# Optimization experiments

Measured on AMD Instinct MI355X. Metric: run time of the kernel, lower is better.

## Reference

```python
import jax, jax.numpy as jnp
import numpy as np

# dims
B, NO, NE = 32, 100, 600          # batch, img objects, img edges
NK, KE, L = 1000, 1000, 8         # kg entities, kg edges, token len
R = 8                              # reasoning-program nodes
H, IMG, LOC = 512, 2048, 5        # hidden, img feat, loc feat
EMB, V, MID, C = 300, 10000, 512, 3000
PAD = 1


def lang_encode(tokens, embed, W, b):
    # masked mean-pool of word embeddings + projection (LanguageEncoder)
    m = (tokens != PAD).astype(jnp.float32)            # [B,N,L]
    e = embed[tokens]                                   # [B,N,L,EMB]
    pooled = (e * m[..., None]).sum(-2) / jnp.maximum(m.sum(-1, keepdims=True), 1.0)
    return jnp.tanh(pooled @ W + b)                     # [B,N,H]


def find_attn(q, k, mask, Wq, Wk, v):
    # Find module: additive attention of program-node queries over key set
    qp = q @ Wq                                         # [B,R,MID]
    kp = k @ Wk                                         # [B,N,MID]
    s = jnp.einsum('brnm,m->brn', jnp.tanh(qp[:, :, None, :] + kp[:, None, :, :]), v)
    if mask is not None:
        s = jnp.where(mask[:, None, :], s, -1e9)
    return jax.nn.softmax(s, axis=-1)                   # [B,R,N] attention maps


def setup_inputs():
    key = jax.random.key(0)
    ks = jax.random.split(key, 30)
    w = lambda i, shp: jax.random.normal(ks[i], shp, jnp.float32) * 0.05
    inp = {
        'img_feat': jax.random.normal(ks[0], (B, NO, IMG), jnp.float32),
        'img_loc': jax.random.uniform(ks[1], (B, NO, LOC), jnp.float32),
        'img_node1_id_list': jax.random.randint(ks[2], (B, NE), 0, NO),
        'img_node2_id_list': jax.random.randint(ks[3], (B, NE), 0, NO),
        'kg_entity': jax.random.randint(ks[4], (B, NK, L), 0, V),
        'kg_e1_ids_list': jax.random.randint(ks[5], (B, KE), 0, NK),
        'kg_e2_ids_list': jax.random.randint(ks[6], (B, KE), 0, NK),
        'kg_edge': jax.random.randint(ks[7], (B, KE, L), 0, V),
        'r_nodes': jax.random.randint(ks[8], (B, R, L), 0, V),
        'r_connects': jax.random.randint(ks[9], (B, R), 0, R),
        'r_type': jax.random.randint(ks[10], (B, R), 0, 3),
        'embed': w(11, (V, EMB)),
        'W_lang': w(12, (EMB, H)), 'b_lang': jnp.zeros((H,), jnp.float32),
        'W_img': w(13, (IMG, H)), 'b_img': jnp.zeros((H,), jnp.float32),
        'W_loc': w(14, (LOC, H)), 'b_loc': jnp.zeros((H,), jnp.float32),
        'W_rel': w(15, (2 * H, H)), 'b_rel': jnp.zeros((H,), jnp.float32),
        'Wq_n': w(16, (H, MID)), 'Wk_n': w(17, (H, MID)), 'v_n': w(18, (MID,)),
        'Wq_e': w(19, (H, MID)), 'Wk_e': w(20, (H, MID)), 'v_e': w(21, (MID,)),
        'W1': w(22, (H, MID)), 'b1': jnp.zeros((MID,), jnp.float32),
        'W2': w(23, (MID, C)), 'b2': jnp.zeros((C,), jnp.float32),
    }
    return inp


def reference(img_feat, img_loc, img_node1_id_list, img_node2_id_list, kg_entity,
              kg_e1_ids_list, kg_e2_ids_list, kg_edge, r_nodes, r_connects, r_type,
              embed, W_lang, b_lang, W_img, b_img, W_loc, b_loc, W_rel, b_rel,
              Wq_n, Wk_n, v_n, Wq_e, Wk_e, v_e, W1, b1, W2, b2):
    # --- image graph features ---
    img_f = img_feat @ W_img + b_img                    # [B,NO,H]
    img_node_feat = img_f + (img_loc @ W_loc + b_loc)
    n1 = jnp.take_along_axis(img_f, img_node1_id_list[..., None], axis=1)  # [B,NE,H]
    n2 = jnp.take_along_axis(img_f, img_node2_id_list[..., None], axis=1)
    img_edge_feat = jnp.concatenate([n1, n2], -1) @ W_rel + b_rel          # [B,NE,H]
    # --- kg graph features ---
    kg_node_feat = lang_encode(kg_entity, embed, W_lang, b_lang)           # [B,NK,H]
    kg_node_mask = jnp.any(kg_entity != PAD, axis=-1)                      # [B,NK]
    kg_edge_feat = lang_encode(kg_edge, embed, W_lang, b_lang)             # [B,KE,H]
    # --- reasoning-program node features ---
    r_feat = lang_encode(r_nodes, embed, W_lang, b_lang)                   # [B,R,H]
    # --- Find over nodes (img + kg entities) ---
    node_keys = jnp.concatenate([img_node_feat, kg_node_feat], axis=1)     # [B,NO+NK,H]
    node_mask = jnp.concatenate([jnp.ones((B, NO), bool), kg_node_mask], axis=1)
    all_map = find_attn(r_feat, node_keys, node_mask, Wq_n, Wk_n, v_n)     # [B,R,NO+NK]
    node_re = jnp.einsum('brn,bnh->brh', all_map, node_keys)               # grounded node feats
    # --- Find over edges (img + kg relations) ---
    edge_keys = jnp.concatenate([img_edge_feat, kg_edge_feat], axis=1)     # [B,NE+KE,H]
    edge_map = find_attn(r_feat, edge_keys, None, Wq_e, Wk_e, v_e)
    edge_ctx = jnp.einsum('brn,bnh->brh', edge_map, edge_keys)
    # --- Reason head on root program node ---
    final = node_re[:, -1] + edge_ctx[:, -1]                               # [B,H]
    return jnp.tanh(final @ W1 + b1) @ W2 + b2                             # [B,C]
```

## Files before the change

kernel.cpp:

```cpp
#include <hip/hip_runtime.h>
#include <hip/hip_bf16.h>
#include <math.h>

#define B_   32
#define NO_  100
#define NE_  600
#define NK_  1000
#define KE_  1000
#define L_   8
#define R_   8
#define H_   512
#define IMG_ 2048
#define LOC_ 5
#define EMB_ 300
#define MID_ 512
#define C_   3000
#define PAD_ 1

#define NN_  (NO_ + NK_)
#define NEK_ (NE_ + KE_)

typedef __attribute__((ext_vector_type(8))) short bf16x8;
typedef __attribute__((ext_vector_type(4))) float f32x4;

__device__ __forceinline__ float4 ldf4(const float* p) { return *(const float4*)p; }

__device__ __forceinline__ float bf2f(short s) {
    unsigned u = ((unsigned)(unsigned short)s) << 16;
    float f; __builtin_memcpy(&f, &u, 4); return f;
}
__device__ __forceinline__ short f2bf(float f) {
    unsigned u; __builtin_memcpy(&u, &f, 4);
    u = (u + 0x7fffu + ((u >> 16) & 1u)) >> 16;
    return (short)u;
}

__device__ __forceinline__ long tiled_off(int row, int k, int KSa) {
    return ((((long)(row >> 7) * KSa + (k >> 5)) * 4 + ((k >> 3) & 3)) << 10)
           + ((long)(row & 127) << 3) + (k & 7);
}

__device__ __forceinline__ void gload16(const void* g, void* l) {
    __builtin_amdgcn_global_load_lds(
        (__attribute__((address_space(1))) void*)(g),
        (__attribute__((address_space(3))) void*)(l), 16, 0, 0);
}

__global__ __launch_bounds__(256) void wprep_kernel(
    const float* __restrict__ W, short* __restrict__ Wp, int K, int KS)
{
    int idx = blockIdx.x * 256 + threadIdx.x;
    int total = 4 * KS * 4 * 128;
    if (idx >= total) return;
    int nl = idx & 127;
    int kg = (idx >> 7) & 3;
    int t  = idx >> 9;
    int ks = t % KS;
    int nb = t / KS;
    int n = nb * 128 + nl;
    short o[8];
#pragma unroll
    for (int j = 0; j < 8; ++j) {
        int k = ks * 32 + kg * 8 + j;
        o[j] = (k < K) ? f2bf(W[(long)k * H_ + n]) : (short)0;
    }
    *(uint4*)&Wp[(long)idx * 8] = *(uint4*)o;
}

__global__ __launch_bounds__(256) void cvt_bf16_kernel(
    const float* __restrict__ src, short* __restrict__ dst, long n)
{
    long i = ((long)blockIdx.x * 256 + threadIdx.x) * 8;
    if (i >= n) return;
    float4 a = ldf4(src + i), b = ldf4(src + i + 4);
    short o[8] = { f2bf(a.x), f2bf(a.y), f2bf(a.z), f2bf(a.w),
                   f2bf(b.x), f2bf(b.y), f2bf(b.z), f2bf(b.w) };
    *(uint4*)&dst[i] = *(uint4*)o;
}

__global__ __launch_bounds__(256) void cvt_tiled_kernel(
    const float* __restrict__ src, short* __restrict__ dst, int K, long ngroups)
{
    long g = (long)blockIdx.x * 256 + threadIdx.x;
    if (g >= ngroups) return;
    int perRow = K >> 3;
    int row = (int)(g / perRow);
    int k   = (int)(g - (long)row * perRow) * 8;
    const float* p = src + (long)row * K + k;
    float4 a = ldf4(p), b = ldf4(p + 4);
    short o[8] = { f2bf(a.x), f2bf(a.y), f2bf(a.z), f2bf(a.w),
                   f2bf(b.x), f2bf(b.y), f2bf(b.z), f2bf(b.w) };
    *(uint4*)&dst[tiled_off(row, k, K >> 5)] = *(uint4*)o;
}

__global__ __launch_bounds__(256) void pool_kernel(
    const int* __restrict__ tokA, const int* __restrict__ tokB, int split,
    int tok_stride, int tok_off, const short* __restrict__ embed_bf,
    short* __restrict__ pooled, float* __restrict__ maskout, int nrows)
{
    __shared__ int   toks[32][8];
    __shared__ float rinv[32];
    int tid = threadIdx.x, base = blockIdx.x * 32;
    const int* tokens; int local;
    if (base < split) { tokens = tokA; local = base; }
    else              { tokens = tokB; local = base - split; }
    {
        int r = tid >> 3, t = tid & 7;
        int i = base + r;
        toks[r][t] = (i < nrows) ? tokens[tok_off + (long)(local + r) * tok_stride + t] : PAD_;
    }
    __syncthreads();
    if (tid < 32) {
        int c = 0;
#pragma unroll
        for (int t = 0; t < 8; ++t) c += (toks[tid][t] != PAD_);
        rinv[tid] = 1.0f / fmaxf((float)c, 1.0f);
        int i = base + tid;
        if (maskout && i < split && i < nrows) maskout[i] = (c > 0) ? 1.0f : 0.0f;
    }
    __syncthreads();

    for (int task = tid; task < 32 * 40; task += 256) {
        int r = task / 40, kg = task - r * 40;
        float s[8] = {0.f,0.f,0.f,0.f,0.f,0.f,0.f,0.f};
        if (kg < 38) {
#pragma unroll
            for (int t = 0; t < 8; ++t) {
                int tok = toks[r][t];
                if (tok != PAD_) {
                    bf16x8 e = *(const bf16x8*)&embed_bf[(long)tok * EMB_ + kg * 8];
#pragma unroll
                    for (int j = 0; j < 8; ++j) s[j] += bf2f(e[j]);
                }
            }
        }
        float iv = rinv[r];
        short o[8];
#pragma unroll
        for (int j = 0; j < 8; ++j) {
            float v = s[j] * iv;
            if (kg == 37 && j >= 4) v = 0.f;
            o[j] = f2bf(v);
        }
        *(uint4*)&pooled[tiled_off(base + r, kg * 8, 10)] = *(uint4*)o;
    }
}

template<int DUAL>
__global__ __launch_bounds__(256) void keys_gemm_kernel(
    const short* __restrict__ Atl, const short* __restrict__ Wp,
    const float* __restrict__ bias,
    short* __restrict__ node_tl, short* __restrict__ edge_tl,
    float* __restrict__ outf, int nrows)
{
    const int NCH = 5;
    __shared__ __align__(16) short As[8192];
    __shared__ __align__(16) short Bs[8192];
    int tid = threadIdx.x;
    int m0 = blockIdx.x * 128, nb = blockIdx.y, n0 = nb * 128;
    int w = tid >> 6, l = tid & 63, wr = w >> 1, wc = w & 1;
    const short* wslab = Wp + (long)nb * (NCH * 2) * 4096;
    const short* aslab0 = Atl + (long)blockIdx.x * (NCH * 2) * 4096;

    f32x4 acc[4][4];
#pragma unroll
    for (int m = 0; m < 4; ++m)
#pragma unroll
        for (int n = 0; n < 4; ++n)
#pragma unroll
            for (int k = 0; k < 4; ++k) acc[m][n][k] = 0.f;

    int kg = l >> 4, li = l & 15;
    for (int t = 0; t < NCH; ++t) {
        const short* aslab = aslab0 + (long)(t * 2) * 4096;
        const short* bslab = wslab + (long)(t * 2) * 4096;
#pragma unroll
        for (int j = 0; j < 4; ++j) {
            int c = w * 4 + j;
            gload16(aslab + c * 512 + l * 8, As + c * 512);
            gload16(bslab + c * 512 + l * 8, Bs + c * 512);
        }
        __syncthreads();
#pragma unroll
        for (int s = 0; s < 2; ++s) {
            bf16x8 af[4], bfr[4];
#pragma unroll
            for (int m = 0; m < 4; ++m)
                af[m] = *(const bf16x8*)&As[(s * 4 + kg) * 1024 + (wr * 64 + m * 16 + li) * 8];
#pragma unroll
            for (int n = 0; n < 4; ++n)
                bfr[n] = *(const bf16x8*)&Bs[(s * 4 + kg) * 1024 + (wc * 64 + n * 16 + li) * 8];
#pragma unroll
            for (int m = 0; m < 4; ++m)
#pragma unroll
                for (int n = 0; n < 4; ++n)
                    acc[m][n] = __builtin_amdgcn_mfma_f32_16x16x32_bf16(af[m], bfr[n], acc[m][n], 0, 0, 0);
        }
        __syncthreads();
    }

    int jrow4 = (l >> 4) * 4;
    float bv[4];
#pragma unroll
    for (int n = 0; n < 4; ++n) bv[n] = bias[n0 + wc * 64 + n * 16 + li];
#pragma unroll
    for (int m = 0; m < 4; ++m)
#pragma unroll
        for (int j = 0; j < 4; ++j) {
            int i = m0 + wr * 64 + m * 16 + jrow4 + j;
            if (i >= nrows) continue;
#pragma unroll
            for (int n = 0; n < 4; ++n) {
                int col = n0 + wc * 64 + n * 16 + li;
                float val = tanhf(acc[m][n][j] + bv[n]);
                if (DUAL) {
                    if (i < B_ * NK_) {
                        int b = i / NK_, k = i - b * NK_;
                        long gr = (long)b * NN_ + NO_ + k;
                        node_tl[tiled_off((int)gr, col, 16)] = f2bf(val);
                    } else {
                        int i2 = i - B_ * NK_;
                        int b = i2 / KE_, k = i2 - b * KE_;
                        long gr = (long)b * NEK_ + NE_ + k;
                        edge_tl[tiled_off((int)gr, col, 16)] = f2bf(val);
                    }
                } else {
                    outf[(long)i * H_ + col] = val;
                }
            }
        }
}

template<int AV, int EP, int NCH>
__global__ __launch_bounds__(256) void mfma_gemm_kernel(
    const short* __restrict__ A, const short* __restrict__ Wp,
    const int* __restrict__ id1, const int* __restrict__ id2,
    const short* __restrict__ Agather,
    const float* __restrict__ bias, const float* __restrict__ bias2,
    const float* __restrict__ loc, const float* __restrict__ Wloc,
    const float* __restrict__ qp, const float* __restrict__ vvec,
    short* __restrict__ out0, short* __restrict__ out1,
    float* __restrict__ sout, int Nrows, int Mtot)
{
    __shared__ __align__(16) short As[8192];
    __shared__ __align__(16) short Bs[8192];
    int tid = threadIdx.x;
    int m0 = blockIdx.x * 128, nb = blockIdx.y, n0 = nb * 128;
    int w = tid >> 6, l = tid & 63, wr = w >> 1, wc = w & 1;

    int r1[2], r2[2];
    if (AV == 2) {
#pragma unroll
        for (int i = 0; i < 2; ++i) {
            int row = m0 + i * 64 + l;
            int b = row / NE_;
            r1[i] = b * NO_ + id1[row];
            r2[i] = b * NO_ + id2[row];
        }
    }
    const short* wslab = Wp + (long)nb * (NCH * 2) * 4096;
    const short* aslab0 = (AV == 3) ? A + (long)blockIdx.x * (NCH * 2) * 4096 : nullptr;

    f32x4 acc[4][4];
#pragma unroll
    for (int m = 0; m < 4; ++m)
#pragma unroll
        for (int n = 0; n < 4; ++n)
#pragma unroll
            for (int k = 0; k < 4; ++k) acc[m][n][k] = 0.f;

    int kg = l >> 4, li = l & 15;
    for (int t = 0; t < NCH; ++t) {
        const short* bslab = wslab + (long)(t * 2) * 4096;
#pragma unroll
        for (int j = 0; j < 4; ++j) {
            int c = w * 4 + j;
            if (AV == 3) {
                gload16(aslab0 + (long)(t * 2) * 4096 + c * 512 + l * 8, As + c * 512);
            } else {
                int g = c >> 1, h2 = c & 1;
                int kk = t * 64 + g * 8;
                int row = (kk < 512) ? r1[h2] : r2[h2];
                gload16(Agather + (long)row * 512 + (kk & 511), As + c * 512);
            }
            gload16(bslab + c * 512 + l * 8, Bs + c * 512);
        }
        __syncthreads();
#pragma unroll
        for (int s = 0; s < 2; ++s) {
            bf16x8 af[4], bfr[4];
#pragma unroll
            for (int m = 0; m < 4; ++m)
                af[m] = *(const bf16x8*)&As[(s * 4 + kg) * 1024 + (wr * 64 + m * 16 + li) * 8];
#pragma unroll
            for (int n = 0; n < 4; ++n)
                bfr[n] = *(const bf16x8*)&Bs[(s * 4 + kg) * 1024 + (wc * 64 + n * 16 + li) * 8];
#pragma unroll
            for (int m = 0; m < 4; ++m)
#pragma unroll
                for (int n = 0; n < 4; ++n)
                    acc[m][n] = __builtin_amdgcn_mfma_f32_16x16x32_bf16(af[m], bfr[n], acc[m][n], 0, 0, 0);
        }
        __syncthreads();
    }

    int jrow4 = (l >> 4) * 4;
    if (EP == 0) {
        float bi[4], bl[4], wl[4][5];
#pragma unroll
        for (int n = 0; n < 4; ++n) {
            int col = n0 + wc * 64 + n * 16 + li;
            bi[n] = bias[col]; bl[n] = bias2[col];
#pragma unroll
            for (int j5 = 0; j5 < 5; ++j5) wl[n][j5] = Wloc[j5 * H_ + col];
        }
#pragma unroll
        for (int m = 0; m < 4; ++m)
#pragma unroll
            for (int j = 0; j < 4; ++j) {
                int row = m0 + wr * 64 + m * 16 + jrow4 + j;
                int b = row / NO_, o = row - b * NO_;
                float lv[5];
#pragma unroll
                for (int j5 = 0; j5 < 5; ++j5) lv[j5] = loc[(long)row * 5 + j5];
                long gr = (long)b * NN_ + o;
#pragma unroll
                for (int n = 0; n < 4; ++n) {
                    int col = n0 + wc * 64 + n * 16 + li;
                    float val = acc[m][n][j] + bi[n];
                    out0[(long)row * H_ + col] = f2bf(val);
                    float nk = val + bl[n];
#pragma unroll
                    for (int j5 = 0; j5 < 5; ++j5) nk = fmaf(lv[j5], wl[n][j5], nk);
                    out1[tiled_off((int)gr, col, 16)] = f2bf(nk);
                }
            }
    } else if (EP == 1) {
        float bi[4];
#pragma unroll
        for (int n = 0; n < 4; ++n) bi[n] = bias[n0 + wc * 64 + n * 16 + li];
#pragma unroll
        for (int m = 0; m < 4; ++m)
#pragma unroll
            for (int j = 0; j < 4; ++j) {
                int row = m0 + wr * 64 + m * 16 + jrow4 + j;
                int b = row / NE_, e = row - b * NE_;
                long gr = (long)b * NEK_ + e;
#pragma unroll
                for (int n = 0; n < 4; ++n) {
                    int col = n0 + wc * 64 + n * 16 + li;
                    out0[tiled_off((int)gr, col, 16)] = f2bf(acc[m][n][j] + bi[n]);
                }
            }
    } else {
        float vv[4];
        int cols[4];
#pragma unroll
        for (int n = 0; n < 4; ++n) {
            cols[n] = n0 + wc * 64 + n * 16 + li;
            vv[n] = vvec[cols[n]];
        }
        int slot = nb * 2 + wc;
#pragma unroll
        for (int m = 0; m < 4; ++m)
#pragma unroll
            for (int j = 0; j < 4; ++j) {
                int row = m0 + wr * 64 + m * 16 + jrow4 + j;
                int b = row / Nrows;
                const float* qpb = qp + (long)b * H_;
                float p = 0.f;
#pragma unroll
                for (int n = 0; n < 4; ++n)
                    p += tanhf(qpb[cols[n]] + acc[m][n][j]) * vv[n];
                p += __shfl_xor(p, 1); p += __shfl_xor(p, 2);
                p += __shfl_xor(p, 4); p += __shfl_xor(p, 8);
                if (li == 0) sout[(long)slot * Mtot + row] = p;
            }
    }
}

__global__ __launch_bounds__(256) void softmax_w_kernel(
    const float* __restrict__ sp_n, const float* __restrict__ sp_e,
    const float* __restrict__ maskbuf, float* __restrict__ wn, float* __restrict__ we)
{
    __shared__ float sw[NEK_];
    __shared__ float red[256];
    int b = blockIdx.x, tid = threadIdx.x, set = blockIdx.y;
    const float* sp = set ? sp_e : sp_n;
    float* wout = set ? we : wn;
    int N = set ? NEK_ : NN_;
    long Mtot = set ? (long)B_ * NEK_ : (long)B_ * NN_;

    float lmax = -3.0e38f;
    for (int n = tid; n < N; n += 256) {
        long row = (long)b * N + n;
        float x = 0.f;
#pragma unroll
        for (int s = 0; s < 8; ++s) x += sp[(long)s * Mtot + row];
        if (!set && n >= NO_ && maskbuf[(long)b * NK_ + (n - NO_)] == 0.f) x = -1e30f;
        sw[n] = x;
        lmax = fmaxf(lmax, x);
    }
    red[tid] = lmax; __syncthreads();
    for (int st = 128; st > 0; st >>= 1) {
        if (tid < st) red[tid] = fmaxf(red[tid], red[tid + st]);
        __syncthreads();
    }
    float mx = red[0]; __syncthreads();

    float lsum = 0.f;
    for (int n = tid; n < N; n += 256) {
        float e = expf(sw[n] - mx);
        sw[n] = e;
        lsum += e;
    }
    red[tid] = lsum; __syncthreads();
    for (int st = 128; st > 0; st >>= 1) {
        if (tid < st) red[tid] += red[tid + st];
        __syncthreads();
    }
    float invZ = 1.0f / red[0];
    __syncthreads();
    for (int n = tid; n < N; n += 256)
        wout[(long)b * N + n] = sw[n] * invZ;
}

template<int SP>
__global__ __launch_bounds__(256) void wsum_kernel(
    const float* __restrict__ w, const short* __restrict__ keys_tl,
    float* __restrict__ partial, int N)
{
    __shared__ float red[4][512];
    int b = blockIdx.x, sp = blockIdx.y, tid = threadIdx.x;
    int c8 = (tid & 63) * 8, rsub = tid >> 6;
    int per = (N + SP - 1) / SP;
    int n0 = sp * per, n1 = min(n0 + per, N);
    float acc[8] = {0.f,0.f,0.f,0.f,0.f,0.f,0.f,0.f};
    for (int n = n0 + rsub; n < n1; n += 4) {
        float wv = w[(long)b * N + n];
        bf16x8 k = *(const bf16x8*)&keys_tl[tiled_off(b * N + n, c8, 16)];
#pragma unroll
        for (int j = 0; j < 8; ++j) acc[j] = fmaf(wv, bf2f(k[j]), acc[j]);
    }
    *(float4*)&red[rsub][c8]     = *(float4*)acc;
    *(float4*)&red[rsub][c8 + 4] = *(float4*)(acc + 4);
    __syncthreads();
    if (rsub == 0) {
        float o[8];
#pragma unroll
        for (int j = 0; j < 8; ++j)
            o[j] = red[0][c8 + j] + red[1][c8 + j] + red[2][c8 + j] + red[3][c8 + j];
        float* op = &partial[((long)sp * B_ + b) * H_ + c8];
        *(float4*)op       = *(float4*)o;
        *(float4*)(op + 4) = *(float4*)(o + 4);
    }
}

__global__ __launch_bounds__(256) void fin_reduce_kernel(
    const float* __restrict__ pn, const float* __restrict__ pe, float* __restrict__ fin)
{
    int i = blockIdx.x * 256 + threadIdx.x;
    float s = 0.f;
#pragma unroll
    for (int sp = 0; sp < 16; ++sp)
        s += pn[(long)sp * B_ * H_ + i] + pe[(long)sp * B_ * H_ + i];
    fin[i] = s;
}

template<int E, int CHUNK>
__global__ __launch_bounds__(256) void kmatvec_kernel(
    const float* __restrict__ in, const float* __restrict__ Wa,
    const float* __restrict__ Wb, float* __restrict__ pa,
    float* __restrict__ pb, int C)
{
    __shared__ float ins[32 * CHUNK];
    int tid = threadIdx.x;
    int ks = blockIdx.y, k0 = ks * CHUNK;
    const float* W   = (blockIdx.z == 0) ? Wa : Wb;
    float* partial   = (blockIdx.z == 0) ? pa : pb;
    for (int t = tid; t < 32 * CHUNK; t += 256) {
        int b = t / CHUNK, k = t - b * CHUNK;
        ins[t] = in[(long)b * E + k0 + k];
    }
    __syncthreads();
    int c = blockIdx.x * 256 + tid;
    if (c >= C) return;
    float acc[32];
#pragma unroll
    for (int b = 0; b < 32; ++b) acc[b] = 0.f;
    for (int k = 0; k < CHUNK; ++k) {
        float wv = W[(long)(k0 + k) * C + c];
#pragma unroll
        for (int b = 0; b < 32; ++b)
            acc[b] = fmaf(ins[b * CHUNK + k], wv, acc[b]);
    }
#pragma unroll
    for (int b = 0; b < 32; ++b)
        partial[((long)ks * 32 + b) * C + c] = acc[b];
}

template<int ACT, int KS>
__global__ __launch_bounds__(256) void kreduce_kernel(
    const float* __restrict__ pa, const float* __restrict__ pb,
    const float* __restrict__ biasa, const float* __restrict__ biasb,
    float* __restrict__ oa, float* __restrict__ ob, int C)
{
    int set = blockIdx.y;
    const float* p    = set ? pb : pa;
    const float* bias = set ? biasb : biasa;
    float* o          = set ? ob : oa;
    long i = (long)blockIdx.x * 256 + threadIdx.x;
    if (i >= 32L * C) return;
    int c = (int)(i % C);
    float s = bias ? bias[c] : 0.f;
#pragma unroll
    for (int ks = 0; ks < KS; ++ks) s += p[(long)ks * 32 * C + i];
    o[i] = (ACT == 1) ? tanhf(s) : s;
}

extern "C" void kernel_launch(void* const* d_in, const int* in_sizes, int n_in,
                              void* d_out, int out_size, void* d_ws, size_t ws_size,
                              hipStream_t stream)
{
    (void)in_sizes; (void)n_in; (void)out_size; (void)ws_size;

    const float* img_feat  = (const float*)d_in[0];
    const float* img_loc   = (const float*)d_in[1];
    const int*   id1       = (const int*)d_in[2];
    const int*   id2       = (const int*)d_in[3];
    const int*   kg_entity = (const int*)d_in[4];
    const int*   kg_edge   = (const int*)d_in[7];
    const int*   r_nodes   = (const int*)d_in[8];
    const float* embed     = (const float*)d_in[11];
    const float* W_lang    = (const float*)d_in[12];
    const float* b_lang    = (const float*)d_in[13];
    const float* W_img     = (const float*)d_in[14];
    const float* b_img     = (const float*)d_in[15];
    const float* W_loc     = (const float*)d_in[16];
    const float* b_loc     = (const float*)d_in[17];
    const float* W_rel     = (const float*)d_in[18];
    const float* b_rel     = (const float*)d_in[19];
    const float* Wq_n      = (const float*)d_in[20];
    const float* Wk_n      = (const float*)d_in[21];
    const float* v_n       = (const float*)d_in[22];
    const float* Wq_e      = (const float*)d_in[23];
    const float* Wk_e      = (const float*)d_in[24];
    const float* v_e       = (const float*)d_in[25];
    const float* W1        = (const float*)d_in[26];
    const float* b1        = (const float*)d_in[27];
    const float* W2        = (const float*)d_in[28];
    const float* b2        = (const float*)d_in[29];
    float* out = (float*)d_out;

    char* ws = (char*)d_ws;
    size_t off = 0;
    auto allocS = [&](size_t n) { short* p = (short*)(ws + off); off += ((n * 2 + 255) & ~255ULL); return p; };
    auto allocF = [&](size_t n) { float* p = (float*)(ws + off); off += ((n * 4 + 255) & ~255ULL); return p; };

    short* img_feat_tl = allocS((size_t)B_ * NO_ * IMG_);
    short* embed_bf    = allocS((size_t)10000 * EMB_ + 16);
    short* Wp_img      = allocS((size_t)4 * 64 * 4096);
    short* Wp_rel      = allocS((size_t)4 * 32 * 4096);
    short* Wp_kn       = allocS((size_t)4 * 16 * 4096);
    short* Wp_ke       = allocS((size_t)4 * 16 * 4096);
    short* Wp_lang     = allocS((size_t)4 * 10 * 4096);
    short* img_f_bf    = allocS((size_t)B_ * NO_ * H_);
    short* node_tl     = allocS((size_t)B_ * NN_ * H_);
    short* edge_tl     = allocS((size_t)B_ * NEK_ * H_);
    short* pooled      = allocS((size_t)2 * B_ * NK_ * 320);
    short* pooled_r    = allocS((size_t)10 * 4096);
    float* rfeat   = allocF((size_t)B_ * H_);
    float* qp_n    = allocF((size_t)B_ * H_);
    float* qp_e    = allocF((size_t)B_ * H_);
    float* mask_kg = allocF((size_t)B_ * NK_);
    float* sp_n    = allocF((size_t)8 * B_ * NN_);
    float* sp_e    = allocF((size_t)8 * B_ * NEK_);
    float* wn      = allocF((size_t)B_ * NN_);
    float* we      = allocF((size_t)B_ * NEK_);
    float* pn      = allocF((size_t)16 * B_ * H_);
    float* pe      = allocF((size_t)16 * B_ * H_);
    float* fin     = allocF((size_t)B_ * H_);
    float* hid     = allocF((size_t)B_ * H_);
    float* pq_n    = allocF((size_t)16 * B_ * MID_);
    float* pq_e    = allocF((size_t)16 * B_ * MID_);
    float* ph1     = allocF((size_t)16 * B_ * MID_);
    float* ph2     = allocF((size_t)16 * B_ * C_);

    cvt_tiled_kernel<<<(B_ * NO_ * IMG_ / 8 + 255) / 256, 256, 0, stream>>>(
        img_feat, img_feat_tl, IMG_, (long)B_ * NO_ * IMG_ / 8);
    cvt_bf16_kernel<<<(10000 * EMB_ / 8 + 255) / 256, 256, 0, stream>>>(
        embed, embed_bf, (long)10000 * EMB_);
    wprep_kernel<<<512, 256, 0, stream>>>(W_img,  Wp_img,  IMG_, 64);
    wprep_kernel<<<256, 256, 0, stream>>>(W_rel,  Wp_rel,  1024, 32);
    wprep_kernel<<<128, 256, 0, stream>>>(Wk_n,   Wp_kn,   512,  16);
    wprep_kernel<<<128, 256, 0, stream>>>(Wk_e,   Wp_ke,   512,  16);
    wprep_kernel<<< 80, 256, 0, stream>>>(W_lang, Wp_lang, EMB_, 10);

    pool_kernel<<<2 * B_ * NK_ / 32, 256, 0, stream>>>(
        kg_entity, kg_edge, B_ * NK_, L_, 0, embed_bf, pooled, mask_kg, 2 * B_ * NK_);
    pool_kernel<<<1, 256, 0, stream>>>(
        r_nodes, nullptr, 1 << 30, R_ * L_, (R_ - 1) * L_, embed_bf, pooled_r,
        nullptr, B_);

    keys_gemm_kernel<1><<<dim3(2 * B_ * NK_ / 128, 4), 256, 0, stream>>>(
        pooled, Wp_lang, b_lang, node_tl, edge_tl, nullptr, 2 * B_ * NK_);
    keys_gemm_kernel<0><<<dim3(1, 4), 256, 0, stream>>>(
        pooled_r, Wp_lang, b_lang, nullptr, nullptr, rfeat, B_);

    kmatvec_kernel<H_, 32><<<dim3(2, 16, 2), 256, 0, stream>>>(
        rfeat, Wq_n, Wq_e, pq_n, pq_e, MID_);
    kreduce_kernel<0, 16><<<dim3(B_ * MID_ / 256, 2), 256, 0, stream>>>(
        pq_n, pq_e, nullptr, nullptr, qp_n, qp_e, MID_);

    mfma_gemm_kernel<3, 0, 32><<<dim3(B_ * NO_ / 128, 4), 256, 0, stream>>>(
        img_feat_tl, Wp_img, nullptr, nullptr, nullptr,
        b_img, b_loc, img_loc, W_loc, nullptr, nullptr,
        img_f_bf, node_tl, nullptr, 0, 0);
    mfma_gemm_kernel<2, 1, 16><<<dim3(B_ * NE_ / 128, 4), 256, 0, stream>>>(
        nullptr, Wp_rel, id1, id2, img_f_bf,
        b_rel, nullptr, nullptr, nullptr, nullptr, nullptr,
        edge_tl, nullptr, nullptr, 0, 0);

    mfma_gemm_kernel<3, 2, 8><<<dim3(B_ * NN_ / 128, 4), 256, 0, stream>>>(
        node_tl, Wp_kn, nullptr, nullptr, nullptr,
        nullptr, nullptr, nullptr, nullptr, qp_n, v_n,
        nullptr, nullptr, sp_n, NN_, B_ * NN_);
    mfma_gemm_kernel<3, 2, 8><<<dim3(B_ * NEK_ / 128, 4), 256, 0, stream>>>(
        edge_tl, Wp_ke, nullptr, nullptr, nullptr,
        nullptr, nullptr, nullptr, nullptr, qp_e, v_e,
        nullptr, nullptr, sp_e, NEK_, B_ * NEK_);

    softmax_w_kernel<<<dim3(B_, 2), 256, 0, stream>>>(sp_n, sp_e, mask_kg, wn, we);
    wsum_kernel<16><<<dim3(B_, 16), 256, 0, stream>>>(wn, node_tl, pn, NN_);
    wsum_kernel<16><<<dim3(B_, 16), 256, 0, stream>>>(we, edge_tl, pe, NEK_);
    fin_reduce_kernel<<<B_ * H_ / 256, 256, 0, stream>>>(pn, pe, fin);

    kmatvec_kernel<H_, 32><<<dim3(2, 16, 1), 256, 0, stream>>>(
        fin, W1, W1, ph1, ph1, MID_);
    kreduce_kernel<1, 16><<<dim3(B_ * MID_ / 256, 1), 256, 0, stream>>>(
        ph1, ph1, b1, b1, hid, hid, MID_);
    kmatvec_kernel<MID_, 32><<<dim3((C_ + 255) / 256, 16, 1), 256, 0, stream>>>(
        hid, W2, W2, ph2, ph2, C_);
    kreduce_kernel<0, 16><<<dim3((B_ * C_ + 255) / 256, 1), 256, 0, stream>>>(
        ph2, ph2, b2, b2, out, out, C_);
}
```

Baseline: 458.3 us.

## Double-buffer LDS tiles in MFMA GEMM kernels to overlap loads with compute

Both the keys GEMM and the generic MFMA GEMM now hold two LDS buffers for A and B. The next K-chunk is prefetched with direct-to-LDS loads while the current chunk is consumed, using a partial vmcnt wait plus raw barriers in place of __syncthreads. The aim is to hide global load latency behind MFMA work. In exchange, LDS use per block doubles to 64KB, which may cut occupancy, and the manual waitcnt ordering is fragile.

Result: slower. 479.8 us (+4.7%).

```diff
diff --git a/kernel.cpp b/kernel.cpp
--- a/kernel.cpp
+++ b/kernel.cpp
@@ -154,49 +154,65 @@
     float* __restrict__ outf, int nrows)
 {
     const int NCH = 5;
-    __shared__ __align__(16) short As[8192];
-    __shared__ __align__(16) short Bs[8192];
+    __shared__ __align__(16) short As[2 * 8192];
+    __shared__ __align__(16) short Bs[2 * 8192];
     int tid = threadIdx.x;
     int m0 = blockIdx.x * 128, nb = blockIdx.y, n0 = nb * 128;
     int w = tid >> 6, l = tid & 63, wr = w >> 1, wc = w & 1;
     const short* wslab = Wp + (long)nb * (NCH * 2) * 4096;
     const short* aslab0 = Atl + (long)blockIdx.x * (NCH * 2) * 4096;
 
-    f32x4 acc[4][4];
-#pragma unroll
-    for (int m = 0; m < 4; ++m)
-#pragma unroll
-        for (int n = 0; n < 4; ++n)
-#pragma unroll
-            for (int k = 0; k < 4; ++k) acc[m][n][k] = 0.f;
-
-    int kg = l >> 4, li = l & 15;
-    for (int t = 0; t < NCH; ++t) {
+    auto stage = [&](int buf, int t) {
         const short* aslab = aslab0 + (long)(t * 2) * 4096;
         const short* bslab = wslab + (long)(t * 2) * 4096;
+        short* Ad = As + buf * 8192;
+        short* Bd = Bs + buf * 8192;
 #pragma unroll
         for (int j = 0; j < 4; ++j) {
             int c = w * 4 + j;
-            gload16(aslab + c * 512 + l * 8, As + c * 512);
-            gload16(bslab + c * 512 + l * 8, Bs + c * 512);
-        }
-        __syncthreads();
+            gload16(aslab + c * 512 + l * 8, Ad + c * 512);
+            gload16(bslab + c * 512 + l * 8, Bd + c * 512);
+        }
+    };
+
+    f32x4 acc[4][4];
+#pragma unroll
+    for (int m = 0; m < 4; ++m)
+#pragma unroll
+        for (int n = 0; n < 4; ++n)
+#pragma unroll
+            for (int k = 0; k < 4; ++k) acc[m][n][k] = 0.f;
+
+    int kg = l >> 4, li = l & 15;
+    stage(0, 0);
+    for (int t = 0; t < NCH; ++t) {
+        int cur = t & 1;
+        if (t + 1 < NCH) {
+            stage(cur ^ 1, t + 1);
+            asm volatile("s_waitcnt vmcnt(8)" ::: "memory");
+        } else {
+            asm volatile("s_waitcnt vmcnt(0)" ::: "memory");
+        }
+        __builtin_amdgcn_s_barrier();
+        const short* Ab = As + cur * 8192;
+        const short* Bb = Bs + cur * 8192;
 #pragma unroll
         for (int s = 0; s < 2; ++s) {
             bf16x8 af[4], bfr[4];
 #pragma unroll
             for (int m = 0; m < 4; ++m)
-                af[m] = *(const bf16x8*)&As[(s * 4 + kg) * 1024 + (wr * 64 + m * 16 + li) * 8];
+                af[m] = *(const bf16x8*)&Ab[(s * 4 + kg) * 1024 + (wr * 64 + m * 16 + li) * 8];
 #pragma unroll
             for (int n = 0; n < 4; ++n)
-                bfr[n] = *(const bf16x8*)&Bs[(s * 4 + kg) * 1024 + (wc * 64 + n * 16 + li) * 8];
+                bfr[n] = *(const bf16x8*)&Bb[(s * 4 + kg) * 1024 + (wc * 64 + n * 16 + li) * 8];
 #pragma unroll
             for (int m = 0; m < 4; ++m)
 #pragma unroll
                 for (int n = 0; n < 4; ++n)
                     acc[m][n] = __builtin_amdgcn_mfma_f32_16x16x32_bf16(af[m], bfr[n], acc[m][n], 0, 0, 0);
         }
-        __syncthreads();
+        asm volatile("" ::: "memory");
+        __builtin_amdgcn_s_barrier();
     }
 
     int jrow4 = (l >> 4) * 4;
@@ -242,8 +258,8 @@
     short* __restrict__ out0, short* __restrict__ out1,
     float* __restrict__ sout, int Nrows, int Mtot)
 {
-    __shared__ __align__(16) short As[8192];
-    __shared__ __align__(16) short Bs[8192];
+    __shared__ __align__(16) short As[2 * 8192];
+    __shared__ __align__(16) short Bs[2 * 8192];
     int tid = threadIdx.x;
     int m0 = blockIdx.x * 128, nb = blockIdx.y, n0 = nb * 128;
     int w = tid >> 6, l = tid & 63, wr = w >> 1, wc = w & 1;
@@ -261,47 +277,63 @@
     const short* wslab = Wp + (long)nb * (NCH * 2) * 4096;
     const short* aslab0 = (AV == 3) ? A + (long)blockIdx.x * (NCH * 2) * 4096 : nullptr;
 
-    f32x4 acc[4][4];
-#pragma unroll
-    for (int m = 0; m < 4; ++m)
-#pragma unroll
-        for (int n = 0; n < 4; ++n)
-#pragma unroll
-            for (int k = 0; k < 4; ++k) acc[m][n][k] = 0.f;
-
-    int kg = l >> 4, li = l & 15;
-    for (int t = 0; t < NCH; ++t) {
+    auto stage = [&](int buf, int t) {
         const short* bslab = wslab + (long)(t * 2) * 4096;
+        short* Ad = As + buf * 8192;
+        short* Bd = Bs + buf * 8192;
 #pragma unroll
         for (int j = 0; j < 4; ++j) {
             int c = w * 4 + j;
             if (AV == 3) {
-                gload16(aslab0 + (long)(t * 2) * 4096 + c * 512 + l * 8, As + c * 512);
+                gload16(aslab0 + (long)(t * 2) * 4096 + c * 512 + l * 8, Ad + c * 512);
             } else {
                 int g = c >> 1, h2 = c & 1;
                 int kk = t * 64 + g * 8;
                 int row = (kk < 512) ? r1[h2] : r2[h2];
-                gload16(Agather + (long)row * 512 + (kk & 511), As + c * 512);
+                gload16(Agather + (long)row * 512 + (kk & 511), Ad + c * 512);
             }
-            gload16(bslab + c * 512 + l * 8, Bs + c * 512);
-        }
-        __syncthreads();
+            gload16(bslab + c * 512 + l * 8, Bd + c * 512);
+        }
+    };
+
+    f32x4 acc[4][4];
+#pragma unroll
+    for (int m = 0; m < 4; ++m)
+#pragma unroll
+        for (int n = 0; n < 4; ++n)
+#pragma unroll
+            for (int k = 0; k < 4; ++k) acc[m][n][k] = 0.f;
+
+    int kg = l >> 4, li = l & 15;
+    stage(0, 0);
+    for (int t = 0; t < NCH; ++t) {
+        int cur = t & 1;
+        if (t + 1 < NCH) {
+            stage(cur ^ 1, t + 1);
+            asm volatile("s_waitcnt vmcnt(8)" ::: "memory");
+        } else {
+            asm volatile("s_waitcnt vmcnt(0)" ::: "memory");
+        }
+        __builtin_amdgcn_s_barrier();
+        const short* Ab = As + cur * 8192;
+        const short* Bb = Bs + cur * 8192;
 #pragma unroll
         for (int s = 0; s < 2; ++s) {
             bf16x8 af[4], bfr[4];
 #pragma unroll
             for (int m = 0; m < 4; ++m)
-                af[m] = *(const bf16x8*)&As[(s * 4 + kg) * 1024 + (wr * 64 + m * 16 + li) * 8];
+                af[m] = *(const bf16x8*)&Ab[(s * 4 + kg) * 1024 + (wr * 64 + m * 16 + li) * 8];
 #pragma unroll
             for (int n = 0; n < 4; ++n)
-                bfr[n] = *(const bf16x8*)&Bs[(s * 4 + kg) * 1024 + (wc * 64 + n * 16 + li) * 8];
+                bfr[n] = *(const bf16x8*)&Bb[(s * 4 + kg) * 1024 + (wc * 64 + n * 16 + li) * 8];
 #pragma unroll
             for (int m = 0; m < 4; ++m)
 #pragma unroll
                 for (int n = 0; n < 4; ++n)
                     acc[m][n] = __builtin_amdgcn_mfma_f32_16x16x32_bf16(af[m], bfr[n], acc[m][n], 0, 0, 0);
         }
-        __syncthreads();
+        asm volatile("" ::: "memory");
+        __builtin_amdgcn_s_barrier();
     }
 
     int jrow4 = (l >> 4) * 4;
```
